# Kernel optimization log

Measured on AMD Instinct MI355X. Metric: run time of the kernel, lower is better.

The kernel has to match this reference:

```python
import jax, jax.numpy as jnp
import numpy as np

B, F, D, V = 32768, 39, 64, 1000000  # batch, num_factors(fields per row), embed_dim, vocab


def setup_inputs() -> dict:
    key = jax.random.key(0)
    k0, k1, k2, k3 = jax.random.split(key, 4)
    x = jax.random.randint(k0, (B, F), 0, V)
    emb_table = jax.random.normal(k1, (V, D), dtype=jnp.float32) * 0.01
    bias_table = jax.random.normal(k2, (V, 1), dtype=jnp.float32) * 0.01
    field_inter_weights = jax.random.normal(k3, (F, F), dtype=jnp.float32) * 0.01
    w0 = jnp.zeros((1,), dtype=jnp.float32)
    return {"x": x, "emb_table": emb_table, "bias_table": bias_table,
            "field_inter_weights": field_inter_weights, "w0": w0}


def reference(x, emb_table, bias_table, field_inter_weights, w0):
    emb = emb_table[x]                         # (B, F, D)
    biases_sum = bias_table[x][..., 0].sum(1)  # (B,)
    f = emb.shape[1]
    # upper-triangular (i<j) weighted sum of pairwise inner products:
    # sum_{i<j} W[i,j] * <emb_i, emb_j>  == einsum over Gram matrix with masked W
    w_mask = jnp.where(jnp.triu(jnp.ones((f, f), dtype=bool), k=1),
                       field_inter_weights, 0.0)
    gram = jnp.einsum('bid,bjd->bij', emb, emb)          # (B, F, F)
    interactions = jnp.einsum('bij,ij->b', gram, w_mask)  # (B,)
    return w0 + biases_sum + interactions
```

## Files before the change

kernel.cpp:

```cpp
#include <hip/hip_runtime.h>


#define FW_B 32768
#define FW_F 39
#define FW_D 64

__global__ __launch_bounds__(256) void fwfm_kernel(
    const int*   __restrict__ x,
    const float* __restrict__ emb,
    const float* __restrict__ bias,
    const float* __restrict__ W,
    const float* __restrict__ w0,
    float*       __restrict__ out)
{
    const int wave = threadIdx.x >> 6;
    const int lane = threadIdx.x & 63;
    const int row  = blockIdx.x * 4 + wave;
    if (row >= FW_B) return;

    const int xl   = (lane < FW_F) ? lane : (FW_F - 1);
    const int idxv = x[row * FW_F + xl];

    float part = (lane < FW_F) ? bias[(unsigned)idxv] : 0.0f;

    float v[FW_F];
    #pragma unroll
    for (int i = 0; i < FW_F; ++i) {
        const int si = __shfl(idxv, i, 64);
        const unsigned off = (unsigned)si * (unsigned)FW_D + (unsigned)lane;
        v[i] = __builtin_nontemporal_load(emb + off);
    }

    #pragma unroll
    for (int i = 0; i < FW_F - 1; ++i) {
        float s = 0.0f;
        #pragma unroll
        for (int j = i + 1; j < FW_F; ++j)
            s = fmaf(W[i * FW_F + j], v[j], s);
        part = fmaf(v[i], s, part);
    }

    #pragma unroll
    for (int off = 32; off >= 1; off >>= 1)
        part += __shfl_xor(part, off, 64);

    if (lane == 0)
        out[row] = w0[0] + part;
}

extern "C" void kernel_launch(void* const* d_in, const int* in_sizes, int n_in,
                              void* d_out, int out_size, void* d_ws, size_t ws_size,
                              hipStream_t stream) {
    const int*   x    = (const int*)  d_in[0];
    const float* emb  = (const float*)d_in[1];
    const float* bias = (const float*)d_in[2];
    const float* W    = (const float*)d_in[3];
    const float* w0   = (const float*)d_in[4];
    float* out        = (float*)d_out;

    const int rows_per_block = 4;
    const int grid = (FW_B + rows_per_block - 1) / rows_per_block;
    fwfm_kernel<<<grid, 256, 0, stream>>>(x, emb, bias, W, w0, out);
}
```

Baseline: 74.09 us.

## Process four rows per wave with double-buffered embedding gathers

Each wavefront now handles four batch rows instead of one. It keeps two register buffers so the embedding gather for the next row is issued before the pairwise-interaction compute of the current row. The aim is to hide gather latency behind FMA work and to amortise the W loads and launch overhead over more rows. In exchange, register pressure roughly doubles (two 39-float buffers), which may lower occupancy, and the grid has four times fewer blocks.

Result: slower. 82.92 us (+11.9%).

```diff
diff --git a/kernel.cpp b/kernel.cpp
--- a/kernel.cpp
+++ b/kernel.cpp
@@ -4,6 +4,8 @@
 #define FW_B 32768
 #define FW_F 39
 #define FW_D 64
+#define FW_RPW 4
+#define FW_WPB 4
 
 __global__ __launch_bounds__(256) void fwfm_kernel(
     const int*   __restrict__ x,
@@ -15,37 +17,61 @@
 {
     const int wave = threadIdx.x >> 6;
     const int lane = threadIdx.x & 63;
-    const int row  = blockIdx.x * 4 + wave;
-    if (row >= FW_B) return;
+    const int wid  = blockIdx.x * FW_WPB + wave;
+    const int row0 = wid * FW_RPW;
+    if (row0 >= FW_B) return;
 
-    const int xl   = (lane < FW_F) ? lane : (FW_F - 1);
-    const int idxv = x[row * FW_F + xl];
+    const int xl = (lane < FW_F) ? lane : (FW_F - 1);
 
-    float part = (lane < FW_F) ? bias[(unsigned)idxv] : 0.0f;
+    int   idxs[FW_RPW];
+    float bs  [FW_RPW];
+    #pragma unroll
+    for (int k = 0; k < FW_RPW; ++k)
+        idxs[k] = x[(row0 + k) * FW_F + xl];
+    #pragma unroll
+    for (int k = 0; k < FW_RPW; ++k)
+        bs[k] = (lane < FW_F) ? bias[(unsigned)idxs[k]] : 0.0f;
 
-    float v[FW_F];
-    #pragma unroll
-    for (int i = 0; i < FW_F; ++i) {
-        const int si = __shfl(idxv, i, 64);
-        const unsigned off = (unsigned)si * (unsigned)FW_D + (unsigned)lane;
-        v[i] = __builtin_nontemporal_load(emb + off);
+    float va[FW_F], vb[FW_F];
+
+#define FW_GATHER(buf, k)                                                    \
+    {                                                                        \
+        _Pragma("unroll")                                                    \
+        for (int i = 0; i < FW_F; ++i) {                                     \
+            const int si = __shfl(idxs[k], i, 64);                           \
+            const unsigned off = (unsigned)si * (unsigned)FW_D + (unsigned)lane; \
+            buf[i] = __builtin_nontemporal_load(emb + off);                  \
+        }                                                                    \
     }
 
-    #pragma unroll
-    for (int i = 0; i < FW_F - 1; ++i) {
-        float s = 0.0f;
-        #pragma unroll
-        for (int j = i + 1; j < FW_F; ++j)
-            s = fmaf(W[i * FW_F + j], v[j], s);
-        part = fmaf(v[i], s, part);
+#define FW_COMPUTE(buf, k)                                                   \
+    {                                                                        \
+        float part = bs[k];                                                  \
+        _Pragma("unroll")                                                    \
+        for (int i = 0; i < FW_F - 1; ++i) {                                 \
+            float s = 0.0f;                                                  \
+            _Pragma("unroll")                                                \
+            for (int j = i + 1; j < FW_F; ++j)                               \
+                s = fmaf(W[i * FW_F + j], buf[j], s);                        \
+            part = fmaf(buf[i], s, part);                                    \
+        }                                                                    \
+        _Pragma("unroll")                                                    \
+        for (int off = 32; off >= 1; off >>= 1)                              \
+            part += __shfl_xor(part, off, 64);                               \
+        if (lane == 0) out[row0 + (k)] = w0[0] + part;                       \
     }
 
-    #pragma unroll
-    for (int off = 32; off >= 1; off >>= 1)
-        part += __shfl_xor(part, off, 64);
+    FW_GATHER(va, 0)
+    FW_GATHER(vb, 1)
+    FW_COMPUTE(va, 0)
+    FW_GATHER(va, 2)
+    FW_COMPUTE(vb, 1)
+    FW_GATHER(vb, 3)
+    FW_COMPUTE(va, 2)
+    FW_COMPUTE(vb, 3)
 
-    if (lane == 0)
-        out[row] = w0[0] + part;
+#undef FW_GATHER
+#undef FW_COMPUTE
 }
 
 extern "C" void kernel_launch(void* const* d_in, const int* in_sizes, int n_in,
@@ -58,7 +84,7 @@
     const float* w0   = (const float*)d_in[4];
     float* out        = (float*)d_out;
 
-    const int rows_per_block = 4;
+    const int rows_per_block = FW_WPB * FW_RPW;
     const int grid = (FW_B + rows_per_block - 1) / rows_per_block;
     fwfm_kernel<<<grid, 256, 0, stream>>>(x, emb, bias, W, w0, out);
 }
```
